# Performance work log

Measured on AMD Instinct MI355X. Metric: run time of the kernel, lower is better.

## Reference

```python
import jax, jax.numpy as jnp
import numpy as np

EPS = 1e-8  # torch F.cosine_similarity eps


def setup_inputs() -> dict:
    key = jax.random.key(0)
    x = jax.random.normal(key, (16, 256, 2048), dtype=jnp.float32)
    return {"x": x}


def reference(x) -> jnp.ndarray:
    # x: [b, c, p]. Pairwise cosine similarity between point columns, diag = 1.
    # Equivalent to the original O(p) loop of F.cosine_similarity calls,
    # fused into one batched matmul.
    b, c, p = x.shape
    dots = jnp.einsum("bcp,bcq->bpq", x, x)            # [b, p, p]
    norms = jnp.sqrt(jnp.sum(x * x, axis=1))            # [b, p]
    denom = jnp.maximum(norms[:, :, None] * norms[:, None, :], EPS)
    sim = dots / denom
    eye = jnp.eye(p, dtype=x.dtype)
    res = jnp.where(eye[None, :, :] > 0, jnp.ones((), x.dtype), sim)
    return res
```

## Files before the change

### kernel.cpp

```cpp
#include <hip/hip_runtime.h>

#define B_ 16
#define C_ 256
#define P_ 2048
#define BK 32
#define NT 136
#define NT_OFF 120

typedef __attribute__((ext_vector_type(8))) short short8;
typedef __attribute__((ext_vector_type(4))) float floatx4;

__device__ inline short f2bf(float v) {
  union { float f; unsigned u; } c; c.f = v;
  unsigned r = c.u + 0x7fffu + ((c.u >> 16) & 1u);
  return (short)(r >> 16);
}

#define GLOAD_LDS16(g, l)                                          \
  __builtin_amdgcn_global_load_lds(                                \
      (const __attribute__((address_space(1))) void*)(g),          \
      (__attribute__((address_space(3))) void*)(l), 16, 0, 0)

__global__ __launch_bounds__(256, 4) void k_transpose(const float* __restrict__ x,
                                                      short* __restrict__ Xt,
                                                      float* __restrict__ nrm2) {
  __shared__ float t[32][33];
  __shared__ float red[8][32];
  const int p0 = blockIdx.x * 32, b = blockIdx.y;
  const float* xb = x + (size_t)b * C_ * P_;
  short* xtb = Xt + (size_t)b * P_ * C_;
  const int tx = threadIdx.x, ty = threadIdx.y;
  const int tid = ty * 32 + tx;
  const int r = tid >> 3, ch = tid & 7;
  float s = 0.f;
#pragma unroll 1
  for (int ci = 0; ci < 8; ++ci) {
    const int c0 = ci * 32;
#pragma unroll
    for (int i = 0; i < 4; ++i) {
      float v = xb[(size_t)(c0 + ty + i * 8) * P_ + p0 + tx];
      t[ty + i * 8][tx] = v;
      s += v * v;
    }
    __syncthreads();
    short4 w;
    w.x = f2bf(t[ch * 4 + 0][r]);
    w.y = f2bf(t[ch * 4 + 1][r]);
    w.z = f2bf(t[ch * 4 + 2][r]);
    w.w = f2bf(t[ch * 4 + 3][r]);
    *reinterpret_cast<short4*>(&xtb[(size_t)(p0 + r) * C_ + c0 + ch * 4]) = w;
    __syncthreads();
  }
  red[ty][tx] = s;
  __syncthreads();
  if (tid < 32) {
    float ns = 0.f;
#pragma unroll
    for (int j = 0; j < 8; ++j) ns += red[j][tid];
    nrm2[b * P_ + p0 + tid] = ns;
  }
}

__global__ __launch_bounds__(256, 3) void k_gemm(const short* __restrict__ Xt,
                                                 const float* __restrict__ nrm2,
                                                 float* __restrict__ out) {
  const int bid = blockIdx.x;
  const int xcd = bid & 7;
  const int s = bid >> 3;
  const int b = xcd * 2 + (s >= NT);
  int t = s - (s >= NT ? NT : 0);

  int tm, tn;
  if (t < NT_OFF) {
    int rem = t, len = 15;
    tm = 0;
    while (rem >= len) { rem -= len; --len; ++tm; }
    tn = tm + 1 + rem;
  } else {
    tm = tn = t - NT_OFF;
  }
  const int p0 = tm * 128, q0 = tn * 128;
  const short* Xb = Xt + (size_t)b * P_ * C_;

  __shared__ __align__(16) char smem[32768];

  const int tid = threadIdx.x;
  const int lane = tid & 63;
  const int wid = tid >> 6;
  const int wrow = wid >> 1;
  const int wcol = wid & 1;

  floatx4 acc[4][4];
#pragma unroll
  for (int i = 0; i < 4; ++i)
#pragma unroll
    for (int j = 0; j < 4; ++j) acc[i][j] = (floatx4){0.f, 0.f, 0.f, 0.f};

  const int K2 = C_ * 2;

  auto STAGE = [&](int buf, int kt) {
    const int kb = kt * (BK * 2);
#pragma unroll
    for (int j = 0; j < 2; ++j) {
      const int chunk = j * 4 + wid;
      const int f = chunk * 1024 + lane * 16;
      const int row = f >> 6;
      const int inrow = f & 63;
      GLOAD_LDS16((const char*)Xb + (size_t)(p0 + row) * K2 + kb + inrow,
                  smem + buf * 8192 + chunk * 1024);
      GLOAD_LDS16((const char*)Xb + (size_t)(q0 + row) * K2 + kb + inrow,
                  smem + 16384 + buf * 8192 + chunk * 1024);
    }
  };

  STAGE(0, 0);

  for (int kt = 0; kt < C_ / BK; ++kt) {
    const int cur = kt & 1;
    if (kt < C_ / BK - 1) {
      STAGE(cur ^ 1, kt + 1);
      asm volatile("s_waitcnt vmcnt(4)\n\ts_barrier" ::: "memory");
    } else {
      asm volatile("s_waitcnt vmcnt(0)\n\ts_barrier" ::: "memory");
    }

    const short* As = (const short*)(smem + cur * 8192);
    const short* Bs = (const short*)(smem + 16384 + cur * 8192);
    short8 af[4], bf[4];
#pragma unroll
    for (int mi = 0; mi < 4; ++mi) {
      const int r = wrow * 64 + mi * 16 + (lane & 15);
      af[mi] = *reinterpret_cast<const short8*>(&As[r * BK + (lane >> 4) * 8]);
    }
#pragma unroll
    for (int ni = 0; ni < 4; ++ni) {
      const int r = wcol * 64 + ni * 16 + (lane & 15);
      bf[ni] = *reinterpret_cast<const short8*>(&Bs[r * BK + (lane >> 4) * 8]);
    }
#pragma unroll
    for (int mi = 0; mi < 4; ++mi)
#pragma unroll
      for (int ni = 0; ni < 4; ++ni)
        acc[mi][ni] = __builtin_amdgcn_mfma_f32_16x16x32_bf16(af[mi], bf[ni], acc[mi][ni], 0, 0, 0);

    asm volatile("s_waitcnt lgkmcnt(0)\n\ts_barrier" ::: "memory");
  }

  const float* n2 = nrm2 + (size_t)b * P_;
  float* ob = out + (size_t)b * P_ * P_;
  const int cl = lane & 15, rg4 = (lane >> 4) * 4;

  float rnq[4];
#pragma unroll
  for (int ni = 0; ni < 4; ++ni) {
    const int qc = q0 + wcol * 64 + ni * 16 + cl;
    rnq[ni] = __builtin_amdgcn_rcpf(fmaxf(sqrtf(n2[qc]), 1e-4f));
  }
  floatx4 rnp[4];
#pragma unroll
  for (int mi = 0; mi < 4; ++mi) {
    const float4 p2 = *reinterpret_cast<const float4*>(&n2[p0 + wrow * 64 + mi * 16 + rg4]);
    rnp[mi][0] = __builtin_amdgcn_rcpf(fmaxf(sqrtf(p2.x), 1e-4f));
    rnp[mi][1] = __builtin_amdgcn_rcpf(fmaxf(sqrtf(p2.y), 1e-4f));
    rnp[mi][2] = __builtin_amdgcn_rcpf(fmaxf(sqrtf(p2.z), 1e-4f));
    rnp[mi][3] = __builtin_amdgcn_rcpf(fmaxf(sqrtf(p2.w), 1e-4f));
  }

  float* etile = (float*)smem + wid * 1280;

#pragma unroll
  for (int mi = 0; mi < 4; ++mi) {
    const int prow = p0 + wrow * 64 + mi * 16 + rg4;
#pragma unroll
    for (int ni = 0; ni < 4; ++ni) {
      floatx4 vv = acc[mi][ni] * rnp[mi] * rnq[ni];
      const int qc = q0 + wcol * 64 + ni * 16 + cl;
      if (tm == tn) {
        const int d = qc - prow;
        if (d >= 0 && d < 4) vv[d] = 1.0f;
      }
      ob[(size_t)(prow + 0) * P_ + qc] = vv[0];
      ob[(size_t)(prow + 1) * P_ + qc] = vv[1];
      ob[(size_t)(prow + 2) * P_ + qc] = vv[2];
      ob[(size_t)(prow + 3) * P_ + qc] = vv[3];
      if (tm != tn)
        *reinterpret_cast<floatx4*>(&etile[(ni * 16 + cl) * 20 + rg4]) = vv;
    }
    if (tm != tn) {
      const int pcb = p0 + wrow * 64 + mi * 16;
#pragma unroll
      for (int i = 0; i < 4; ++i) {
        const int qq = i * 16 + (lane >> 2);
        const floatx4 mv = *reinterpret_cast<const floatx4*>(&etile[qq * 20 + (lane & 3) * 4]);
        *reinterpret_cast<floatx4*>(
            &ob[(size_t)(q0 + wcol * 64 + qq) * P_ + pcb + (lane & 3) * 4]) = mv;
      }
    }
  }
}

extern "C" void kernel_launch(void* const* d_in, const int* in_sizes, int n_in,
                              void* d_out, int out_size, void* d_ws, size_t ws_size,
                              hipStream_t stream) {
  const float* x = (const float*)d_in[0];
  float* out = (float*)d_out;

  short* Xt = (short*)d_ws;
  float* nrm2 = (float*)((char*)d_ws + (size_t)B_ * P_ * C_ * sizeof(short));

  k_transpose<<<dim3(P_ / 32, B_), dim3(32, 8), 0, stream>>>(x, Xt, nrm2);
  k_gemm<<<dim3(NT * B_), 256, 0, stream>>>(Xt, nrm2, out);
}
```

Baseline: 82.55 us.

## Triple-buffer GEMM loads, widen transpose kernel, use nontemporal output stores

Switches the GEMM K-loop from double to triple buffering in LDS so two stages of global-to-LDS loads are in flight, at the cost of more shared memory per block. Reworks the transpose kernel to handle 128 points per block with float4 loads and splits channels across two z-blocks, writing partial squared norms that the GEMM epilogue sums. Output stores become nontemporal to reduce cache pollution on the large output write.

```diff
diff --git a/kernel.cpp b/kernel.cpp
--- a/kernel.cpp
+++ b/kernel.cpp
@@ -4,6 +4,7 @@
 #define C_ 256
 #define P_ 2048
 #define BK 32
+#define KT 8
 #define NT 136
 #define NT_OFF 120
 
@@ -23,46 +24,59 @@
 
 __global__ __launch_bounds__(256, 4) void k_transpose(const float* __restrict__ x,
                                                       short* __restrict__ Xt,
-                                                      float* __restrict__ nrm2) {
-  __shared__ float t[32][33];
-  __shared__ float red[8][32];
-  const int p0 = blockIdx.x * 32, b = blockIdx.y;
+                                                      float* __restrict__ nrm2p) {
+  __shared__ float t[32][133];
+  __shared__ float red[8][32][4];
+  const int p0 = blockIdx.x * 128, b = blockIdx.y, zc = blockIdx.z;
   const float* xb = x + (size_t)b * C_ * P_;
   short* xtb = Xt + (size_t)b * P_ * C_;
-  const int tx = threadIdx.x, ty = threadIdx.y;
-  const int tid = ty * 32 + tx;
-  const int r = tid >> 3, ch = tid & 7;
-  float s = 0.f;
+  const int tid = threadIdx.x;
+  const int tx = tid & 31;
+  const int cg = tid >> 5;
+  floatx4 s4 = (floatx4){0.f, 0.f, 0.f, 0.f};
+  const int cbase = zc * 128;
 #pragma unroll 1
-  for (int ci = 0; ci < 8; ++ci) {
-    const int c0 = ci * 32;
+  for (int chunk = 0; chunk < 4; ++chunk) {
+    const int c0 = cbase + chunk * 32;
+    float4 v[4];
+#pragma unroll
+    for (int i = 0; i < 4; ++i)
+      v[i] = *reinterpret_cast<const float4*>(&xb[(size_t)(c0 + cg + i * 8) * P_ + p0 + tx * 4]);
 #pragma unroll
     for (int i = 0; i < 4; ++i) {
-      float v = xb[(size_t)(c0 + ty + i * 8) * P_ + p0 + tx];
-      t[ty + i * 8][tx] = v;
-      s += v * v;
+      *reinterpret_cast<float4*>(&t[cg + i * 8][tx * 4]) = v[i];
+      s4[0] += v[i].x * v[i].x;
+      s4[1] += v[i].y * v[i].y;
+      s4[2] += v[i].z * v[i].z;
+      s4[3] += v[i].w * v[i].w;
     }
     __syncthreads();
-    short4 w;
-    w.x = f2bf(t[ch * 4 + 0][r]);
-    w.y = f2bf(t[ch * 4 + 1][r]);
-    w.z = f2bf(t[ch * 4 + 2][r]);
-    w.w = f2bf(t[ch * 4 + 3][r]);
-    *reinterpret_cast<short4*>(&xtb[(size_t)(p0 + r) * C_ + c0 + ch * 4]) = w;
+#pragma unroll
+    for (int u = 0; u < 4; ++u) {
+      const int unit = tid + 256 * u;
+      const int r = unit >> 3, ch = unit & 7;
+      short4 w;
+      w.x = f2bf(t[ch * 4 + 0][r]);
+      w.y = f2bf(t[ch * 4 + 1][r]);
+      w.z = f2bf(t[ch * 4 + 2][r]);
+      w.w = f2bf(t[ch * 4 + 3][r]);
+      *reinterpret_cast<short4*>(&xtb[(size_t)(p0 + r) * C_ + c0 + ch * 4]) = w;
+    }
     __syncthreads();
   }
-  red[ty][tx] = s;
+  *reinterpret_cast<floatx4*>(&red[cg][tx][0]) = s4;
   __syncthreads();
-  if (tid < 32) {
+  if (tid < 128) {
+    const int cgp = tid >> 2, j = tid & 3;
     float ns = 0.f;
 #pragma unroll
-    for (int j = 0; j < 8; ++j) ns += red[j][tid];
-    nrm2[b * P_ + p0 + tid] = ns;
+    for (int g = 0; g < 8; ++g) ns += red[g][cgp][j];
+    nrm2p[(size_t)zc * B_ * P_ + b * P_ + p0 + tid] = ns;
   }
 }
 
 __global__ __launch_bounds__(256, 3) void k_gemm(const short* __restrict__ Xt,
-                                                 const float* __restrict__ nrm2,
+                                                 const float* __restrict__ nrm2p,
                                                  float* __restrict__ out) {
   const int bid = blockIdx.x;
   const int xcd = bid & 7;
@@ -82,7 +96,7 @@
   const int p0 = tm * 128, q0 = tn * 128;
   const short* Xb = Xt + (size_t)b * P_ * C_;
 
-  __shared__ __align__(16) char smem[32768];
+  __shared__ __align__(16) char smem[49152];
 
   const int tid = threadIdx.x;
   const int lane = tid & 63;
@@ -107,25 +121,26 @@
       const int row = f >> 6;
       const int inrow = f & 63;
       GLOAD_LDS16((const char*)Xb + (size_t)(p0 + row) * K2 + kb + inrow,
-                  smem + buf * 8192 + chunk * 1024);
+                  smem + buf * 16384 + chunk * 1024);
       GLOAD_LDS16((const char*)Xb + (size_t)(q0 + row) * K2 + kb + inrow,
-                  smem + 16384 + buf * 8192 + chunk * 1024);
+                  smem + buf * 16384 + 8192 + chunk * 1024);
     }
   };
 
   STAGE(0, 0);
-
-  for (int kt = 0; kt < C_ / BK; ++kt) {
-    const int cur = kt & 1;
-    if (kt < C_ / BK - 1) {
-      STAGE(cur ^ 1, kt + 1);
+  STAGE(1, 1);
+
+  for (int kt = 0; kt < KT; ++kt) {
+    if (kt < KT - 1) {
       asm volatile("s_waitcnt vmcnt(4)\n\ts_barrier" ::: "memory");
     } else {
       asm volatile("s_waitcnt vmcnt(0)\n\ts_barrier" ::: "memory");
     }
-
-    const short* As = (const short*)(smem + cur * 8192);
-    const short* Bs = (const short*)(smem + 16384 + cur * 8192);
+    if (kt + 2 < KT) STAGE((kt + 2) % 3, kt + 2);
+
+    const int cur = kt % 3;
+    const short* As = (const short*)(smem + cur * 16384);
+    const short* Bs = (const short*)(smem + cur * 16384 + 8192);
     short8 af[4], bf[4];
 #pragma unroll
     for (int mi = 0; mi < 4; ++mi) {
@@ -146,7 +161,8 @@
     asm volatile("s_waitcnt lgkmcnt(0)\n\ts_barrier" ::: "memory");
   }
 
-  const float* n2 = nrm2 + (size_t)b * P_;
+  const float* n2a = nrm2p + (size_t)b * P_;
+  const float* n2b = nrm2p + (size_t)B_ * P_ + (size_t)b * P_;
   float* ob = out + (size_t)b * P_ * P_;
   const int cl = lane & 15, rg4 = (lane >> 4) * 4;
 
@@ -154,16 +170,18 @@
 #pragma unroll
   for (int ni = 0; ni < 4; ++ni) {
     const int qc = q0 + wcol * 64 + ni * 16 + cl;
-    rnq[ni] = __builtin_amdgcn_rcpf(fmaxf(sqrtf(n2[qc]), 1e-4f));
+    rnq[ni] = __builtin_amdgcn_rcpf(fmaxf(sqrtf(n2a[qc] + n2b[qc]), 1e-4f));
   }
   floatx4 rnp[4];
 #pragma unroll
   for (int mi = 0; mi < 4; ++mi) {
-    const float4 p2 = *reinterpret_cast<const float4*>(&n2[p0 + wrow * 64 + mi * 16 + rg4]);
-    rnp[mi][0] = __builtin_amdgcn_rcpf(fmaxf(sqrtf(p2.x), 1e-4f));
-    rnp[mi][1] = __builtin_amdgcn_rcpf(fmaxf(sqrtf(p2.y), 1e-4f));
-    rnp[mi][2] = __builtin_amdgcn_rcpf(fmaxf(sqrtf(p2.z), 1e-4f));
-    rnp[mi][3] = __builtin_amdgcn_rcpf(fmaxf(sqrtf(p2.w), 1e-4f));
+    const int pb = p0 + wrow * 64 + mi * 16 + rg4;
+    const float4 pa = *reinterpret_cast<const float4*>(&n2a[pb]);
+    const float4 pbv = *reinterpret_cast<const float4*>(&n2b[pb]);
+    rnp[mi][0] = __builtin_amdgcn_rcpf(fmaxf(sqrtf(pa.x + pbv.x), 1e-4f));
+    rnp[mi][1] = __builtin_amdgcn_rcpf(fmaxf(sqrtf(pa.y + pbv.y), 1e-4f));
+    rnp[mi][2] = __builtin_amdgcn_rcpf(fmaxf(sqrtf(pa.z + pbv.z), 1e-4f));
+    rnp[mi][3] = __builtin_amdgcn_rcpf(fmaxf(sqrtf(pa.w + pbv.w), 1e-4f));
   }
 
   float* etile = (float*)smem + wid * 1280;
@@ -179,10 +197,10 @@
         const int d = qc - prow;
         if (d >= 0 && d < 4) vv[d] = 1.0f;
       }
-      ob[(size_t)(prow + 0) * P_ + qc] = vv[0];
-      ob[(size_t)(prow + 1) * P_ + qc] = vv[1];
-      ob[(size_t)(prow + 2) * P_ + qc] = vv[2];
-      ob[(size_t)(prow + 3) * P_ + qc] = vv[3];
+      __builtin_nontemporal_store(vv[0], &ob[(size_t)(prow + 0) * P_ + qc]);
+      __builtin_nontemporal_store(vv[1], &ob[(size_t)(prow + 1) * P_ + qc]);
+      __builtin_nontemporal_store(vv[2], &ob[(size_t)(prow + 2) * P_ + qc]);
+      __builtin_nontemporal_store(vv[3], &ob[(size_t)(prow + 3) * P_ + qc]);
       if (tm != tn)
         *reinterpret_cast<floatx4*>(&etile[(ni * 16 + cl) * 20 + rg4]) = vv;
     }
@@ -192,8 +210,9 @@
       for (int i = 0; i < 4; ++i) {
         const int qq = i * 16 + (lane >> 2);
         const floatx4 mv = *reinterpret_cast<const floatx4*>(&etile[qq * 20 + (lane & 3) * 4]);
-        *reinterpret_cast<floatx4*>(
-            &ob[(size_t)(q0 + wcol * 64 + qq) * P_ + pcb + (lane & 3) * 4]) = mv;
+        __builtin_nontemporal_store(
+            mv, reinterpret_cast<floatx4*>(
+                    &ob[(size_t)(q0 + wcol * 64 + qq) * P_ + pcb + (lane & 3) * 4]));
       }
     }
   }
@@ -206,8 +225,8 @@
   float* out = (float*)d_out;
 
   short* Xt = (short*)d_ws;
-  float* nrm2 = (float*)((char*)d_ws + (size_t)B_ * P_ * C_ * sizeof(short));
-
-  k_transpose<<<dim3(P_ / 32, B_), dim3(32, 8), 0, stream>>>(x, Xt, nrm2);
-  k_gemm<<<dim3(NT * B_), 256, 0, stream>>>(Xt, nrm2, out);
-}
+  float* nrm2p = (float*)((char*)d_ws + (size_t)B_ * P_ * C_ * sizeof(short));
+
+  k_transpose<<<dim3(P_ / 128, B_, 2), 256, 0, stream>>>(x, Xt, nrm2p);
+  k_gemm<<<dim3(NT * B_), 256, 0, stream>>>(Xt, nrm2p, out);
+}
```

After: 105.1 us. 1.27x slower.
